# Performance work log

Hardware: AMD Instinct MI355X
Metric: run time of the kernel (lower is better)

Reference implementation:

```python
import jax, jax.numpy as jnp
import numpy as np

PATCH = 3  # patch_sizes[layer] == 3 for all layers
EPS_NORM = 1e-12   # F.normalize eps
EPS_DIV = 1e-8     # fold divisor eps


def _extract_patches(f, p):
    # F.unfold(kernel=p, stride=1, padding=p//2) -> (b, N=h*w, c, p, p)
    b, c, h, w = f.shape
    pad = p // 2
    xp = jnp.pad(f, ((0, 0), (0, 0), (pad, pad), (pad, pad)))
    # stack the p*p shifted views: (b, c, p*p, h, w)
    pats = jnp.stack([xp[:, :, i:i + h, j:j + w]
                      for i in range(p) for j in range(p)], axis=2)
    # -> (b, c, p, p, N) -> (b, N, c, p, p), matching unfold's (c, kh, kw) ordering
    return pats.reshape(b, c, p, p, h * w).transpose(0, 4, 1, 2, 3)


def _fold(patches, h, w, p):
    # F.fold inverse of unfold: scatter-add overlapping patches.
    # patches: (b, N=h*w, c, p, p)
    b, n, c = patches.shape[:3]
    pad = p // 2
    m = patches.reshape(b, h, w, c, p, p).transpose(0, 3, 4, 5, 1, 2)  # (b,c,p,p,h,w)
    out = jnp.zeros((b, c, h + 2 * pad, w + 2 * pad), patches.dtype)
    for ki in range(p):
        for kj in range(p):
            out = out.at[:, :, ki:ki + h, kj:kj + w].add(m[:, :, ki, kj])
    return out[:, :, pad:pad + h, pad:pad + w]


def _mrf_loss(content_feats, style_feats, p):
    b, c, h, w = content_feats.shape
    d = c * p * p
    cp = _extract_patches(content_feats, p)            # (b, N, c, p, p)
    sp = _extract_patches(style_feats, p)              # (b, M, c, p, p)
    cv = cp.reshape(b, -1, d)
    sv = sp.reshape(b, -1, d)
    cv = cv / jnp.maximum(jnp.linalg.norm(cv, axis=2, keepdims=True), EPS_NORM)
    svn = sv / jnp.maximum(jnp.linalg.norm(sv, axis=2, keepdims=True), EPS_NORM)
    # cosine similarity matrix (b, N, M) -- the big memory-bound intermediate
    dist = jnp.einsum('bnd,bmd->bnm', cv, svn)
    best = jnp.argmax(dist, axis=2)                    # (b, N) int
    # gather matched (un-normalized) style patches
    matched = jnp.take_along_axis(sp.reshape(b, -1, d), best[:, :, None], axis=1)
    matched = matched.reshape(b, -1, c, p, p)
    out = _fold(matched, h, w, p)
    ones = jnp.ones((1, h * w, 1, p, p), content_feats.dtype)
    divisor = _fold(ones, h, w, p)                      # overlap counts (1,1,h,w)
    recon = out / (divisor + EPS_DIV)
    return jnp.mean((content_feats - recon) ** 2)


def setup_inputs() -> dict:
    key = jax.random.key(0)
    k1, k2 = jax.random.split(key)
    content_feats = jax.random.normal(k1, (1, 128, 96, 96), dtype=jnp.float32)
    style_feats = jax.random.normal(k2, (1, 128, 96, 96), dtype=jnp.float32)
    return {"content_feats": content_feats, "style_feats": style_feats}


def reference(content_feats, style_feats):
    return _mrf_loss(content_feats, style_feats, PATCH)
```

## Files before the change

### kernel.cpp

```cpp
#include <hip/hip_runtime.h>
#include <hip/hip_bf16.h>

#define HH 96
#define WW 96
#define NPIX 9216
#define NCH 128
#define DDIM 1152
#define TOTAL_ELEMS 1179648
#define CG 32
#define DDIAG 9217
#define DROW 884832

#define NTIL 8
#define MTIL 512
#define BROWS 10
#define BCOLS 528
#define BELEMS (BROWS * BCOLS)
#define DCHUNKS 1980
#define NTB 1152
#define DBLK 20736

typedef float f32x4 __attribute__((ext_vector_type(4)));
typedef __bf16 bf16x8 __attribute__((ext_vector_type(8)));
typedef _Float16 half8 __attribute__((ext_vector_type(8)));

__device__ __forceinline__ void gload_lds16(const void* g, void* l) {
  __builtin_amdgcn_global_load_lds((const __attribute__((address_space(1))) void*)g,
                                   (__attribute__((address_space(3))) void*)l, 16, 0, 0);
}


#define GUARD_ELEMS 894064ull
constexpr size_t G_CORE_ELEMS = (size_t)NPIX * NPIX;
constexpr size_t G_TOT_ELEMS = G_CORE_ELEMS + 2ull * GUARD_ELEMS;
constexpr size_t GBYTES = ((G_TOT_ELEMS * 2 + 255) & ~(size_t)255);
constexpr size_t CT_OFF = GBYTES;
constexpr size_t ST2_OFF = CT_OFF + (size_t)NPIX * NCH * 2;
constexpr size_t STYT_OFF = ST2_OFF + (size_t)NPIX * NCH * 2;
constexpr size_t SS_OFF = STYT_OFF + (size_t)NPIX * NCH * 4;
constexpr size_t RN2_OFF = SS_OFF + (size_t)NPIX * 4;
constexpr size_t KEY2_OFF = RN2_OFF + (size_t)NPIX * 4;
constexpr size_t NEED_NEW = KEY2_OFF + (size_t)NPIX * 8;

__global__ __launch_bounds__(256)
void transpose_kernel(const float* __restrict__ style_f, const float* __restrict__ content_f,
                      _Float16* __restrict__ St, _Float16* __restrict__ Ct,
                      float* __restrict__ styT, float* __restrict__ ss) {
  __shared__ float ftile[NCH][97];
  const int y = blockIdx.x;
  const bool is_style = (blockIdx.y == 0);
  const float* f = is_style ? style_f : content_f;
  _Float16* P = is_style ? St : Ct;
  const int tid = threadIdx.x;
  for (int i = tid; i < NCH * WW; i += 256) {
    int c = i / WW, x = i - (i / WW) * WW;
    ftile[c][x] = f[(size_t)c * NPIX + y * WW + x];
  }
  __syncthreads();
  for (int j = tid; j < WW * NCH; j += 256) {
    int x = j >> 7, c = j & 127;
    float v = ftile[c][x];
    P[(size_t)(y * WW + x) * NCH + c] = (_Float16)v;
    if (is_style) styT[(size_t)(y * WW + x) * NCH + c] = v;
  }
  if (is_style && tid < WW) {
    float s = 0.f;
#pragma unroll 8
    for (int c = 0; c < NCH; ++c) { float v = ftile[c][tid]; s = fmaf(v, v, s); }
    ss[y * WW + tid] = s;
  }
}

__global__ __launch_bounds__(256)
void boxnorm_kernel(const float* __restrict__ ss, float* __restrict__ rnorm) {
  int m = blockIdx.x * 256 + threadIdx.x;
  int ym = m / WW, xm = m - (m / WW) * WW;
  float s = 0.f;
#pragma unroll
  for (int di = -1; di <= 1; ++di) {
    int yy = ym + di;
    if (yy < 0 || yy >= HH) continue;
#pragma unroll
    for (int dj = -1; dj <= 1; ++dj) {
      int xx = xm + dj;
      if (xx < 0 || xx >= WW) continue;
      s += ss[yy * WW + xx];
    }
  }
  rnorm[m] = 1.0f / fmaxf(sqrtf(s), 1e-12f);
}

__global__ __launch_bounds__(256, 2)
void ggemm_kernel(const _Float16* __restrict__ Ct, const _Float16* __restrict__ St,
                  unsigned short* __restrict__ Gg) {
  __shared__ char smem[65536];
  const int tid = threadIdx.x;
  const int lane = tid & 63, wid = tid >> 6;
  const int l15 = lane & 15, lg = lane >> 4;
  const int wm = wid >> 1, wn = wid & 1;
  const int n0 = blockIdx.x * 128, m0 = blockIdx.y * 128;

  {
    const int r = tid >> 4, p = tid & 15;
    const int l = p ^ (r & 7);
    const _Float16* sa = Ct + (size_t)(n0 + r) * NCH + l * 8;
    const _Float16* sb = St + (size_t)(m0 + r) * NCH + l * 8;
    char* d = smem + tid * 16;
#pragma unroll
    for (int i = 0; i < 8; ++i) {
      gload_lds16(sa + (size_t)16 * i * NCH, d + 4096 * i);
      gload_lds16(sb + (size_t)16 * i * NCH, d + 32768 + 4096 * i);
    }
  }
  __syncthreads();

  f32x4 acc[4][4];
#pragma unroll
  for (int mf = 0; mf < 4; ++mf)
#pragma unroll
    for (int nf = 0; nf < 4; ++nf) {
      f32x4 z = {0.f, 0.f, 0.f, 0.f};
      acc[mf][nf] = z;
    }

#pragma unroll
  for (int ks = 0; ks < 4; ++ks) {
    half8 af[4], bb[4];
#pragma unroll
    for (int mf = 0; mf < 4; ++mf) {
      int row = wm * 64 + mf * 16 + l15;
      int phys = (ks * 4 + lg) ^ (row & 7);
      af[mf] = __builtin_bit_cast(half8, *(const int4*)(smem + row * 256 + phys * 16));
    }
#pragma unroll
    for (int nf = 0; nf < 4; ++nf) {
      int row = wn * 64 + nf * 16 + l15;
      int phys = (ks * 4 + lg) ^ (row & 7);
      bb[nf] = __builtin_bit_cast(half8, *(const int4*)(smem + 32768 + row * 256 + phys * 16));
    }
#pragma unroll
    for (int mf = 0; mf < 4; ++mf)
#pragma unroll
      for (int nf = 0; nf < 4; ++nf)
        acc[mf][nf] = __builtin_amdgcn_mfma_f32_16x16x32_f16(af[mf], bb[nf], acc[mf][nf], 0, 0, 0);
  }
  __syncthreads();

#pragma unroll
  for (int mf = 0; mf < 4; ++mf)
#pragma unroll
    for (int nf = 0; nf < 4; ++nf)
#pragma unroll
      for (int r = 0; r < 4; ++r) {
        int row = wm * 64 + mf * 16 + lg * 4 + r;
        int col = wn * 64 + nf * 16 + l15;
        *(_Float16*)(smem + (row * 136 + col) * 2) = (_Float16)acc[mf][nf][r];
      }
  __syncthreads();
  const size_t gbase = GUARD_ELEMS + (size_t)n0 * NPIX + m0;
#pragma unroll
  for (int j = 0; j < 8; ++j) {
    int idx = j * 256 + tid;
    int row = idx >> 4, ch = idx & 15;
    int4 v = *(const int4*)(smem + (row * 136 + ch * 8) * 2);
    *(int4*)(Gg + gbase + (size_t)row * NPIX + ch * 8) = v;
  }
}

__global__ __launch_bounds__(256, 5)
void dist_argmax_kernel(const _Float16* __restrict__ Gg, const float* __restrict__ rnorm,
                        unsigned long long* __restrict__ keytab) {
  __shared__ _Float16 lds[3 * BELEMS];
  const int bid = blockIdx.x;
  const int idx = (bid & 7) * (DBLK / 8) + (bid >> 3);
  const int mtb = idx / NTB;
  const int ntb = idx - mtb * NTB;
  const int n0 = ntb * NTIL;
  const int m0 = mtb * MTIL;
  const int tid = threadIdx.x;
  const int w = tid >> 6, lane = tid & 63;

  long flat0[3];
#pragma unroll
  for (int b = 0; b < 3; ++b) {
    int di = b - 1;
    flat0[b] = (long)(n0 + 96 * di - 1) * NPIX + (long)(m0 + 96 * di - 8) + (long)GUARD_ELEMS;
  }
#pragma unroll
  for (int k = 0; k < 8; ++k) {
    int q = k * 256 + tid;
    if (q < DCHUNKS) {
      int b = q / 660;
      int rem = q - b * 660;
      int row = rem / 66;
      int c16 = rem - row * 66;
      gload_lds16(Gg + flat0[b] + (long)row * NPIX + c16 * 8, lds + (size_t)q * 8);
    }
  }
  const int mlane = m0 + lane * 8;
  const int ym = mlane / WW;
  const int x8 = mlane - ym * WW;
  const float me0 = (x8 == 0) ? 0.f : 1.f;
  const float me7 = (x8 == 88) ? 0.f : 1.f;
  const bool myr0 = (ym >= 1), myr2 = (ym <= 94);
  float rnv[8];
  *(f32x4*)(rnv) = *(const f32x4*)(rnorm + mlane);
  *(f32x4*)(rnv + 4) = *(const f32x4*)(rnorm + mlane + 4);
  const int col8 = lane * 8 + 8;
  const _Float16* B0p = lds;
  const _Float16* B1p = lds + BELEMS;
  const _Float16* B2p = lds + 2 * BELEMS;

  asm volatile("s_waitcnt vmcnt(0)" ::: "memory");
  __builtin_amdgcn_s_barrier();

#pragma unroll
  for (int s = 0; s < 2; ++s) {
    const int r = w * 2 + s;
    const int n = n0 + r;
    const int yn = n / WW;
    const int xn = n - yn * WW;
    const float cn0 = (xn >= 1) ? 1.f : 0.f;
    const float cn2 = (xn <= 94) ? 1.f : 0.f;
    const float Bw0 = (myr0 && (yn >= 1)) ? 1.f : 0.f;
    const float Bw2 = (myr2 && (yn <= 94)) ? 1.f : 0.f;
    float d[8];
    {
      const _Float16* bp = B1p + r * BCOLS;
      half8 Vp = *(const half8*)(bp + col8 - 8);
      half8 V0 = *(const half8*)(bp + col8);
      half8 V1 = *(const half8*)(bp + BCOLS + col8);
      half8 V2 = *(const half8*)(bp + 2 * BCOLS + col8);
      half8 Vx = *(const half8*)(bp + 2 * BCOLS + col8 + 8);
      float P = (float)Vp[7];
      float X = (float)Vx[0];
#pragma unroll
      for (int j = 0; j < 8; ++j) d[j] = (float)V1[j];
      d[0] = fmaf(P, cn0 * me0, d[0]);
#pragma unroll
      for (int j = 1; j < 8; ++j) d[j] = fmaf((float)V0[j - 1], cn0, d[j]);
#pragma unroll
      for (int j = 0; j < 7; ++j) d[j] = fmaf((float)V2[j + 1], cn2, d[j]);
      d[7] = fmaf(X, cn2 * me7, d[7]);
    }
    {
      const float wl = Bw0 * cn0, wr = Bw0 * cn2;
      const _Float16* bp = B0p + r * BCOLS;
      half8 Vp = *(const half8*)(bp + col8 - 8);
      half8 V0 = *(const half8*)(bp + col8);
      half8 V1 = *(const half8*)(bp + BCOLS + col8);
      half8 V2 = *(const half8*)(bp + 2 * BCOLS + col8);
      half8 Vx = *(const half8*)(bp + 2 * BCOLS + col8 + 8);
      float P = (float)Vp[7];
      float X = (float)Vx[0];
#pragma unroll
      for (int j = 0; j < 8; ++j) d[j] = fmaf((float)V1[j], Bw0, d[j]);
      d[0] = fmaf(P, wl * me0, d[0]);
#pragma unroll
      for (int j = 1; j < 8; ++j) d[j] = fmaf((float)V0[j - 1], wl, d[j]);
#pragma unroll
      for (int j = 0; j < 7; ++j) d[j] = fmaf((float)V2[j + 1], wr, d[j]);
      d[7] = fmaf(X, wr * me7, d[7]);
    }
    {
      const float wl = Bw2 * cn0, wr = Bw2 * cn2;
      const _Float16* bp = B2p + r * BCOLS;
      half8 Vp = *(const half8*)(bp + col8 - 8);
      half8 V0 = *(const half8*)(bp + col8);
      half8 V1 = *(const half8*)(bp + BCOLS + col8);
      half8 V2 = *(const half8*)(bp + 2 * BCOLS + col8);
      half8 Vx = *(const half8*)(bp + 2 * BCOLS + col8 + 8);
      float P = (float)Vp[7];
      float X = (float)Vx[0];
#pragma unroll
      for (int j = 0; j < 8; ++j) d[j] = fmaf((float)V1[j], Bw2, d[j]);
      d[0] = fmaf(P, wl * me0, d[0]);
#pragma unroll
      for (int j = 1; j < 8; ++j) d[j] = fmaf((float)V0[j - 1], wl, d[j]);
#pragma unroll
      for (int j = 0; j < 7; ++j) d[j] = fmaf((float)V2[j + 1], wr, d[j]);
      d[7] = fmaf(X, wr * me7, d[7]);
    }
    float bv = d[0] * rnv[0];
    int bj = mlane;
#pragma unroll
    for (int j = 1; j < 8; ++j) {
      float xs = d[j] * rnv[j];
      if (xs > bv) { bv = xs; bj = mlane + j; }
    }
    float wmx = bv;
#pragma unroll
    for (int mm = 1; mm < 64; mm <<= 1)
      wmx = fmaxf(wmx, __shfl_xor(wmx, mm, 64));
    if (bv == wmx) {
      unsigned u = __float_as_uint(bv);
      u ^= (unsigned)((int)u >> 31) | 0x80000000u;
      unsigned long long key =
          ((unsigned long long)u << 32) | (unsigned)(0xFFFFFFFFu ^ (unsigned)bj);
      atomicMax(keytab + n, key);
    }
  }
}

__global__ __launch_bounds__(256)
void recon_mse2_kernel(const _Float16* __restrict__ Ct, const float* __restrict__ styT,
                       const unsigned long long* __restrict__ keytab, float* __restrict__ out) {
  const int pix = blockIdx.x * 2 + (threadIdx.x >> 7);
  const int c = threadIdx.x & 127;
  const int y = pix / WW, x = pix - (pix / WW) * WW;
  float sum = 0.f, cnt = 0.f;
#pragma unroll
  for (int ki = 0; ki < 3; ++ki) {
    int yn = y - ki + 1;
    if (yn < 0 || yn >= HH) continue;
#pragma unroll
    for (int kj = 0; kj < 3; ++kj) {
      int xn = x - kj + 1;
      if (xn < 0 || xn >= WW) continue;
      cnt += 1.f;
      int m = (int)(0xFFFFFFFFu ^ (unsigned)(keytab[yn * WW + xn] & 0xFFFFFFFFull));
      int ys = m / WW, xs = m - (m / WW) * WW;
      int sy = ys + ki - 1, sx = xs + kj - 1;
      if (sy >= 0 && sy < HH && sx >= 0 && sx < WW)
        sum += styT[(size_t)(sy * WW + sx) * NCH + c];
    }
  }
  float recon = sum / (cnt + 1e-8f);
  float cv = (float)Ct[(size_t)pix * NCH + c];
  float diff = cv - recon;
  float sq = diff * diff;
#pragma unroll
  for (int m = 32; m > 0; m >>= 1) sq += __shfl_down(sq, m, 64);
  __shared__ float wsum[4];
  int lane = threadIdx.x & 63, w = threadIdx.x >> 6;
  if (lane == 0) wsum[w] = sq;
  __syncthreads();
  if (threadIdx.x == 0)
    atomicAdd(out, (wsum[0] + wsum[1] + wsum[2] + wsum[3]) * (1.0f / (float)TOTAL_ELEMS));
}

__global__ __launch_bounds__(256)
void build_patches_old(const float* __restrict__ style_f, const float* __restrict__ content_f,
                       __bf16* __restrict__ Ps, __bf16* __restrict__ Pc) {
  __shared__ float ftile[CG][3][104];
  const int y = blockIdx.x;
  const int cg = blockIdx.y;
  const bool is_style = (blockIdx.z == 0);
  const float* f = is_style ? style_f : content_f;
  __bf16* P = is_style ? Ps : Pc;
  const int tid = threadIdx.x;
  for (int i = tid; i < CG * 3 * 96; i += 256) {
    int cl = i / 288, rem = i - cl * 288;
    int yy = rem / 96, xx = rem - yy * 96;
    int gy = y + yy - 1;
    float v = (gy >= 0 && gy < HH) ? f[(size_t)(cg * CG + cl) * NPIX + gy * WW + xx] : 0.f;
    ftile[cl][yy][xx] = v;
  }
  __syncthreads();
  for (int j = tid; j < 96 * 36; j += 256) {
    int px = j / 36, wi = j - px * 36;
    bf16x8 tmp;
#pragma unroll
    for (int u = 0; u < 8; ++u) {
      int e = wi * 8 + u;
      int cl = e / 9, t = e - cl * 9;
      int ki = t / 3, kj = t - ki * 3;
      int xx = px + kj - 1;
      float v = (xx >= 0 && xx < WW) ? ftile[cl][ki][xx] : 0.f;
      tmp[u] = (__bf16)v;
    }
    *(bf16x8*)(P + (size_t)(y * WW + px) * DDIM + cg * 288 + wi * 8) = tmp;
  }
}

__global__ __launch_bounds__(256)
void norm_old(const __bf16* __restrict__ Ps, float* __restrict__ rnorm) {
  const int n = blockIdx.x * 4 + (threadIdx.x >> 6);
  const int lane = threadIdx.x & 63;
  const bf16x8* row = (const bf16x8*)(Ps + (size_t)n * DDIM);
  float ss = 0.f;
#pragma unroll
  for (int i = 0; i < 3; ++i) {
    int idx = i * 64 + lane;
    if (idx < 144) {
      bf16x8 v = row[idx];
#pragma unroll
      for (int u = 0; u < 8; ++u) { float x = (float)v[u]; ss += x * x; }
    }
  }
#pragma unroll
  for (int m = 1; m < 64; m <<= 1) ss += __shfl_xor(ss, m, 64);
  if (lane == 0) rnorm[n] = 1.0f / fmaxf(sqrtf(ss), 1e-12f);
}

__global__ __launch_bounds__(256, 2)
void gemm_old(const __bf16* __restrict__ Pc, const __bf16* __restrict__ Ps,
              const float* __restrict__ rnorm, unsigned long long* __restrict__ keytab) {
  __shared__ int4 smem4[4608];
  char* smem = (char*)smem4;
  const int tid = threadIdx.x;
  const int lane = tid & 63;
  const int wid = tid >> 6;
  const int l15 = lane & 15;
  const int lg = lane >> 4;
  const int wm = wid >> 1;
  const int wn = wid & 1;
  const int orig = blockIdx.x;
  const int swz = (orig & 7) * 324 + (orig >> 3);
  const int mt = swz / 72;
  const int nt = swz - mt * 72;
  const int bm0 = mt * 256;
  const int sbase = nt * 128;
  const int srow = tid >> 2;
  const int sg = (tid & 3) ^ ((srow >> 1) & 3);
  const __bf16* pa = Pc + (size_t)(bm0 + srow) * DDIM + sg * 8;
  const __bf16* pb = Ps + (size_t)(sbase + srow) * DDIM + sg * 8;
  const int sdst = tid * 16;
  auto stage = [&](int buf, int kt) {
    char* la = smem + buf * 24576 + sdst;
    const int ko = kt * 32;
#pragma unroll
    for (int i = 0; i < 4; ++i) gload_lds16(pa + (size_t)i * 64 * DDIM + ko, la + i * 4096);
#pragma unroll
    for (int j = 0; j < 2; ++j) gload_lds16(pb + (size_t)j * 64 * DDIM + ko, la + 16384 + j * 4096);
  };
  const int sx = (lg ^ ((l15 >> 1) & 3)) << 4;
  int aoff[8], boff[4];
#pragma unroll
  for (int mf = 0; mf < 8; ++mf) aoff[mf] = (wm * 128 + mf * 16 + l15) * 64 + sx;
#pragma unroll
  for (int nf = 0; nf < 4; ++nf) boff[nf] = 16384 + (wn * 64 + nf * 16 + l15) * 64 + sx;
  f32x4 acc[8][4];
#pragma unroll
  for (int mf = 0; mf < 8; ++mf)
#pragma unroll
    for (int nf = 0; nf < 4; ++nf) {
      f32x4 z = {0.f, 0.f, 0.f, 0.f};
      acc[mf][nf] = z;
    }
  auto compute = [&](int buf) {
    const char* bp = smem + buf * 24576;
    bf16x8 af[8], bfr[4];
#pragma unroll
    for (int mf = 0; mf < 8; ++mf) af[mf] = __builtin_bit_cast(bf16x8, *(const int4*)(bp + aoff[mf]));
#pragma unroll
    for (int nf = 0; nf < 4; ++nf) bfr[nf] = __builtin_bit_cast(bf16x8, *(const int4*)(bp + boff[nf]));
    __builtin_amdgcn_s_setprio(1);
#pragma unroll
    for (int mf = 0; mf < 8; ++mf)
#pragma unroll
      for (int nf = 0; nf < 4; ++nf)
        acc[mf][nf] = __builtin_amdgcn_mfma_f32_16x16x32_bf16(af[mf], bfr[nf], acc[mf][nf], 0, 0, 0);
    __builtin_amdgcn_s_setprio(0);
  };
  stage(0, 0);
  stage(1, 1);
  int sb = 2, cb = 0;
  for (int kt = 0; kt < 34; ++kt) {
    stage(sb, kt + 2);
    sb = (sb == 2) ? 0 : sb + 1;
    asm volatile("s_waitcnt vmcnt(12)" ::: "memory");
    __builtin_amdgcn_s_barrier();
    __builtin_amdgcn_sched_barrier(0);
    compute(cb);
    __builtin_amdgcn_s_barrier();
    cb = (cb == 2) ? 0 : cb + 1;
  }
  asm volatile("s_waitcnt vmcnt(6)" ::: "memory");
  __builtin_amdgcn_s_barrier();
  __builtin_amdgcn_sched_barrier(0);
  compute(cb);
  cb = (cb == 2) ? 0 : cb + 1;
  asm volatile("s_waitcnt vmcnt(0)" ::: "memory");
  __builtin_amdgcn_s_barrier();
  __builtin_amdgcn_sched_barrier(0);
  compute(cb);
  float rn[4];
#pragma unroll
  for (int nf = 0; nf < 4; ++nf) rn[nf] = rnorm[sbase + wn * 64 + nf * 16 + l15];
#pragma unroll
  for (int mf = 0; mf < 8; ++mf)
#pragma unroll
    for (int r = 0; r < 4; ++r) {
      float v = -3.0e38f;
      int bi = 0;
#pragma unroll
      for (int nf = 0; nf < 4; ++nf) {
        float x = acc[mf][nf][r] * rn[nf];
        int col = sbase + wn * 64 + nf * 16 + l15;
        if (x > v) { v = x; bi = col; }
      }
#pragma unroll
      for (int m = 1; m < 16; m <<= 1) {
        float ov = __shfl_xor(v, m, 64);
        int oi = __shfl_xor(bi, m, 64);
        if (ov > v || (ov == v && oi < bi)) { v = ov; bi = oi; }
      }
      if (l15 == 0) {
        int row = bm0 + wm * 128 + mf * 16 + lg * 4 + r;
        unsigned u = __float_as_uint(v);
        u ^= (unsigned)((int)u >> 31) | 0x80000000u;
        unsigned long long key = ((unsigned long long)u << 32) | (unsigned)(0xFFFFFFFFu ^ (unsigned)bi);
        atomicMax(keytab + row, key);
      }
    }
}

__global__ __launch_bounds__(256)
void recon_old(const __bf16* __restrict__ Pc, const __bf16* __restrict__ Ps,
               const unsigned long long* __restrict__ keytab, float* __restrict__ out) {
  const int pix = blockIdx.x * 2 + (threadIdx.x >> 7);
  const int c = threadIdx.x & 127;
  const int y = pix / WW, x = pix - (pix / WW) * WW;
  float sum = 0.f, cnt = 0.f;
#pragma unroll
  for (int ki = 0; ki < 3; ++ki) {
    int yn = y - ki + 1;
    if (yn < 0 || yn >= HH) continue;
#pragma unroll
    for (int kj = 0; kj < 3; ++kj) {
      int xn = x - kj + 1;
      if (xn < 0 || xn >= WW) continue;
      cnt += 1.f;
      int m = (int)(0xFFFFFFFFu ^ (unsigned)(keytab[yn * WW + xn] & 0xFFFFFFFFull));
      sum += (float)Ps[(size_t)m * DDIM + c * 9 + ki * 3 + kj];
    }
  }
  float recon = sum / (cnt + 1e-8f);
  float cv = (float)Pc[(size_t)pix * DDIM + c * 9 + 4];
  float diff = cv - recon;
  float sq = diff * diff;
#pragma unroll
  for (int m = 32; m > 0; m >>= 1) sq += __shfl_down(sq, m, 64);
  __shared__ float wsum[4];
  int lane = threadIdx.x & 63, w = threadIdx.x >> 6;
  if (lane == 0) wsum[w] = sq;
  __syncthreads();
  if (threadIdx.x == 0)
    atomicAdd(out, (wsum[0] + wsum[1] + wsum[2] + wsum[3]) * (1.0f / (float)TOTAL_ELEMS));
}

extern "C" void kernel_launch(void* const* d_in, const int* in_sizes, int n_in,
                              void* d_out, int out_size, void* d_ws, size_t ws_size,
                              hipStream_t stream) {
  const float* content = (const float*)d_in[0];
  const float* stylef = (const float*)d_in[1];
  float* out = (float*)d_out;
  char* ws = (char*)d_ws;

  hipMemsetAsync(d_out, 0, (size_t)out_size * sizeof(float), stream);

  if (ws_size >= NEED_NEW) {
    _Float16* Gg = (_Float16*)ws;
    _Float16* Ct = (_Float16*)(ws + CT_OFF);
    _Float16* St = (_Float16*)(ws + ST2_OFF);
    float* styT = (float*)(ws + STYT_OFF);
    float* ss = (float*)(ws + SS_OFF);
    float* rnorm = (float*)(ws + RN2_OFF);
    unsigned long long* keytab = (unsigned long long*)(ws + KEY2_OFF);

    hipMemsetAsync(keytab, 0, (size_t)NPIX * 8, stream);
    hipMemsetAsync(Gg, 0, (size_t)GUARD_ELEMS * 2, stream);
    hipMemsetAsync(Gg + GUARD_ELEMS + G_CORE_ELEMS, 0, (size_t)GUARD_ELEMS * 2, stream);
    transpose_kernel<<<dim3(96, 2), 256, 0, stream>>>(stylef, content, St, Ct, styT, ss);
    boxnorm_kernel<<<NPIX / 256, 256, 0, stream>>>(ss, rnorm);
    ggemm_kernel<<<dim3(72, 72), 256, 0, stream>>>(Ct, St, (unsigned short*)Gg);
    dist_argmax_kernel<<<DBLK, 256, 0, stream>>>(Gg, rnorm, keytab);
    recon_mse2_kernel<<<NPIX / 2, 256, 0, stream>>>(Ct, styT, keytab, out);
  } else {
    const size_t PS_OFF = 0;
    const size_t PC_OFF = (size_t)NPIX * DDIM * 2;
    const size_t RN_OFF = PC_OFF * 2;
    const size_t KEY_OFF = RN_OFF + (size_t)NPIX * 4;
    __bf16* Ps = (__bf16*)(ws + PS_OFF);
    __bf16* Pc = (__bf16*)(ws + PC_OFF);
    float* rnorm = (float*)(ws + RN_OFF);
    unsigned long long* keytab = (unsigned long long*)(ws + KEY_OFF);
    hipMemsetAsync(keytab, 0, (size_t)NPIX * 8, stream);
    build_patches_old<<<dim3(96, 4, 2), 256, 0, stream>>>(stylef, content, Ps, Pc);
    norm_old<<<NPIX / 4, 256, 0, stream>>>(Ps, rnorm);
    gemm_old<<<2592, 256, 0, stream>>>(Pc, Ps, rnorm, keytab);
    recon_old<<<NPIX / 2, 256, 0, stream>>>(Pc, Ps, keytab, out);
  }
}
```

Baseline: 214.2 us.

## Fold memsets into kernels and share LDS row loads across two output rows

Removes four hipMemsetAsync calls. The keytab and output zeroing now happen inside the transpose kernel, and the guard-band zeroing is spread across the GEMM blocks. The dist_argmax inner loop is restructured so that each wave loads four consecutive LDS rows per band once and reuses them for both of its output rows. Neighbour elements are fetched with lane shuffles instead of extra unaligned LDS loads. This cuts launch overhead and LDS traffic, at the cost of more registers and some shuffle work.

```diff
diff --git a/kernel.cpp b/kernel.cpp
--- a/kernel.cpp
+++ b/kernel.cpp
@@ -28,7 +28,6 @@
   __builtin_amdgcn_global_load_lds((const __attribute__((address_space(1))) void*)g,
                                    (__attribute__((address_space(3))) void*)l, 16, 0, 0);
 }
-
 
 #define GUARD_ELEMS 894064ull
 constexpr size_t G_CORE_ELEMS = (size_t)NPIX * NPIX;
@@ -41,17 +40,24 @@
 constexpr size_t RN2_OFF = SS_OFF + (size_t)NPIX * 4;
 constexpr size_t KEY2_OFF = RN2_OFF + (size_t)NPIX * 4;
 constexpr size_t NEED_NEW = KEY2_OFF + (size_t)NPIX * 8;
+constexpr long GUARD_I4 = 111758;
 
 __global__ __launch_bounds__(256)
 void transpose_kernel(const float* __restrict__ style_f, const float* __restrict__ content_f,
                       _Float16* __restrict__ St, _Float16* __restrict__ Ct,
-                      float* __restrict__ styT, float* __restrict__ ss) {
+                      float* __restrict__ styT, float* __restrict__ ss,
+                      unsigned long long* __restrict__ keytab, float* __restrict__ out) {
   __shared__ float ftile[NCH][97];
   const int y = blockIdx.x;
   const bool is_style = (blockIdx.y == 0);
   const float* f = is_style ? style_f : content_f;
   _Float16* P = is_style ? St : Ct;
   const int tid = threadIdx.x;
+  if (is_style) {
+    int g = y * 256 + tid;
+    if (g < NPIX) keytab[g] = 0ull;
+    if (g == 0) *out = 0.f;
+  }
   for (int i = tid; i < NCH * WW; i += 256) {
     int c = i / WW, x = i - (i / WW) * WW;
     ftile[c][x] = f[(size_t)c * NPIX + y * WW + x];
@@ -101,6 +107,20 @@
   const int n0 = blockIdx.x * 128, m0 = blockIdx.y * 128;
 
   {
+    const long bidf = (long)blockIdx.y * gridDim.x + blockIdx.x;
+    if (tid < 64) {
+      int side = tid >> 5, k = tid & 31;
+      if (k < 22) {
+        long q = bidf * 22 + k;
+        if (q < GUARD_I4) {
+          int4 z = {0, 0, 0, 0};
+          _Float16* gp = (_Float16*)Gg + (side ? (long)(GUARD_ELEMS + G_CORE_ELEMS) : 0l);
+          *(int4*)(gp + q * 8) = z;
+        }
+      }
+    }
+  }
+  {
     const int r = tid >> 4, p = tid & 15;
     const int l = p ^ (r & 7);
     const _Float16* sa = Ct + (size_t)(n0 + r) * NCH + l * 8;
@@ -122,7 +142,6 @@
       f32x4 z = {0.f, 0.f, 0.f, 0.f};
       acc[mf][nf] = z;
     }
-
 #pragma unroll
   for (int ks = 0; ks < 4; ++ks) {
     half8 af[4], bb[4];
@@ -145,7 +164,6 @@
         acc[mf][nf] = __builtin_amdgcn_mfma_f32_16x16x32_f16(af[mf], bb[nf], acc[mf][nf], 0, 0, 0);
   }
   __syncthreads();
-
 #pragma unroll
   for (int mf = 0; mf < 4; ++mf)
 #pragma unroll
@@ -207,97 +225,99 @@
   *(f32x4*)(rnv) = *(const f32x4*)(rnorm + mlane);
   *(f32x4*)(rnv + 4) = *(const f32x4*)(rnorm + mlane + 4);
   const int col8 = lane * 8 + 8;
-  const _Float16* B0p = lds;
-  const _Float16* B1p = lds + BELEMS;
-  const _Float16* B2p = lds + 2 * BELEMS;
+
+  const int r0 = w * 2;
+  const int nA = n0 + r0, nB = nA + 1;
+  const int ynA = nA / WW, xnA = nA - ynA * WW;
+  const int ynB = nB / WW, xnB = nB - ynB * WW;
+  const float cn0A = (xnA >= 1) ? 1.f : 0.f, cn2A = (xnA <= 94) ? 1.f : 0.f;
+  const float cn0B = (xnB >= 1) ? 1.f : 0.f, cn2B = (xnB <= 94) ? 1.f : 0.f;
+  const float bwA[3] = {(myr0 && (ynA >= 1)) ? 1.f : 0.f, 1.f, (myr2 && (ynA <= 94)) ? 1.f : 0.f};
+  const float bwB[3] = {(myr0 && (ynB >= 1)) ? 1.f : 0.f, 1.f, (myr2 && (ynB <= 94)) ? 1.f : 0.f};
 
   asm volatile("s_waitcnt vmcnt(0)" ::: "memory");
   __builtin_amdgcn_s_barrier();
 
-#pragma unroll
-  for (int s = 0; s < 2; ++s) {
-    const int r = w * 2 + s;
-    const int n = n0 + r;
-    const int yn = n / WW;
-    const int xn = n - yn * WW;
-    const float cn0 = (xn >= 1) ? 1.f : 0.f;
-    const float cn2 = (xn <= 94) ? 1.f : 0.f;
-    const float Bw0 = (myr0 && (yn >= 1)) ? 1.f : 0.f;
-    const float Bw2 = (myr2 && (yn <= 94)) ? 1.f : 0.f;
-    float d[8];
+  float dA[8] = {0.f, 0.f, 0.f, 0.f, 0.f, 0.f, 0.f, 0.f};
+  float dB[8] = {0.f, 0.f, 0.f, 0.f, 0.f, 0.f, 0.f, 0.f};
+#pragma unroll
+  for (int b = 0; b < 3; ++b) {
+    const _Float16* bp = lds + b * BELEMS + r0 * BCOLS;
+    half8 R0 = *(const half8*)(bp + col8);
+    half8 R1 = *(const half8*)(bp + BCOLS + col8);
+    half8 R2 = *(const half8*)(bp + 2 * BCOLS + col8);
+    half8 R3 = *(const half8*)(bp + 3 * BCOLS + col8);
+    float pA = __shfl_up((float)R0[7], 1, 64);
+    float pB = __shfl_up((float)R1[7], 1, 64);
+    float xA = __shfl_down((float)R2[0], 1, 64);
+    float xB = __shfl_down((float)R3[0], 1, 64);
+    if (lane == 0) {
+      pA = (float)bp[7];
+      pB = (float)bp[BCOLS + 7];
+    }
+    if (lane == 63) {
+      xA = (float)bp[2 * BCOLS + 520];
+      xB = (float)bp[3 * BCOLS + 520];
+    }
     {
-      const _Float16* bp = B1p + r * BCOLS;
-      half8 Vp = *(const half8*)(bp + col8 - 8);
-      half8 V0 = *(const half8*)(bp + col8);
-      half8 V1 = *(const half8*)(bp + BCOLS + col8);
-      half8 V2 = *(const half8*)(bp + 2 * BCOLS + col8);
-      half8 Vx = *(const half8*)(bp + 2 * BCOLS + col8 + 8);
-      float P = (float)Vp[7];
-      float X = (float)Vx[0];
-#pragma unroll
-      for (int j = 0; j < 8; ++j) d[j] = (float)V1[j];
-      d[0] = fmaf(P, cn0 * me0, d[0]);
-#pragma unroll
-      for (int j = 1; j < 8; ++j) d[j] = fmaf((float)V0[j - 1], cn0, d[j]);
-#pragma unroll
-      for (int j = 0; j < 7; ++j) d[j] = fmaf((float)V2[j + 1], cn2, d[j]);
-      d[7] = fmaf(X, cn2 * me7, d[7]);
+      const float wc = bwA[b];
+      const float wl = wc * cn0A, wr = wc * cn2A;
+#pragma unroll
+      for (int j = 0; j < 8; ++j) dA[j] = fmaf((float)R1[j], wc, dA[j]);
+      dA[0] = fmaf(pA, wl * me0, dA[0]);
+#pragma unroll
+      for (int j = 1; j < 8; ++j) dA[j] = fmaf((float)R0[j - 1], wl, dA[j]);
+#pragma unroll
+      for (int j = 0; j < 7; ++j) dA[j] = fmaf((float)R2[j + 1], wr, dA[j]);
+      dA[7] = fmaf(xA, wr * me7, dA[7]);
     }
     {
-      const float wl = Bw0 * cn0, wr = Bw0 * cn2;
-      const _Float16* bp = B0p + r * BCOLS;
-      half8 Vp = *(const half8*)(bp + col8 - 8);
-      half8 V0 = *(const half8*)(bp + col8);
-      half8 V1 = *(const half8*)(bp + BCOLS + col8);
-      half8 V2 = *(const half8*)(bp + 2 * BCOLS + col8);
-      half8 Vx = *(const half8*)(bp + 2 * BCOLS + col8 + 8);
-      float P = (float)Vp[7];
-      float X = (float)Vx[0];
-#pragma unroll
-      for (int j = 0; j < 8; ++j) d[j] = fmaf((float)V1[j], Bw0, d[j]);
-      d[0] = fmaf(P, wl * me0, d[0]);
-#pragma unroll
-      for (int j = 1; j < 8; ++j) d[j] = fmaf((float)V0[j - 1], wl, d[j]);
-#pragma unroll
-      for (int j = 0; j < 7; ++j) d[j] = fmaf((float)V2[j + 1], wr, d[j]);
-      d[7] = fmaf(X, wr * me7, d[7]);
-    }
-    {
-      const float wl = Bw2 * cn0, wr = Bw2 * cn2;
-      const _Float16* bp = B2p + r * BCOLS;
-      half8 Vp = *(const half8*)(bp + col8 - 8);
-      half8 V0 = *(const half8*)(bp + col8);
-      half8 V1 = *(const half8*)(bp + BCOLS + col8);
-      half8 V2 = *(const half8*)(bp + 2 * BCOLS + col8);
-      half8 Vx = *(const half8*)(bp + 2 * BCOLS + col8 + 8);
-      float P = (float)Vp[7];
-      float X = (float)Vx[0];
-#pragma unroll
-      for (int j = 0; j < 8; ++j) d[j] = fmaf((float)V1[j], Bw2, d[j]);
-      d[0] = fmaf(P, wl * me0, d[0]);
-#pragma unroll
-      for (int j = 1; j < 8; ++j) d[j] = fmaf((float)V0[j - 1], wl, d[j]);
-#pragma unroll
-      for (int j = 0; j < 7; ++j) d[j] = fmaf((float)V2[j + 1], wr, d[j]);
-      d[7] = fmaf(X, wr * me7, d[7]);
-    }
-    float bv = d[0] * rnv[0];
+      const float wc = bwB[b];
+      const float wl = wc * cn0B, wr = wc * cn2B;
+#pragma unroll
+      for (int j = 0; j < 8; ++j) dB[j] = fmaf((float)R2[j], wc, dB[j]);
+      dB[0] = fmaf(pB, wl * me0, dB[0]);
+#pragma unroll
+      for (int j = 1; j < 8; ++j) dB[j] = fmaf((float)R1[j - 1], wl, dB[j]);
+#pragma unroll
+      for (int j = 0; j < 7; ++j) dB[j] = fmaf((float)R3[j + 1], wr, dB[j]);
+      dB[7] = fmaf(xB, wr * me7, dB[7]);
+    }
+  }
+  {
+    float bv = dA[0] * rnv[0];
     int bj = mlane;
 #pragma unroll
     for (int j = 1; j < 8; ++j) {
-      float xs = d[j] * rnv[j];
+      float xs = dA[j] * rnv[j];
       if (xs > bv) { bv = xs; bj = mlane + j; }
     }
     float wmx = bv;
 #pragma unroll
-    for (int mm = 1; mm < 64; mm <<= 1)
-      wmx = fmaxf(wmx, __shfl_xor(wmx, mm, 64));
+    for (int mm = 1; mm < 64; mm <<= 1) wmx = fmaxf(wmx, __shfl_xor(wmx, mm, 64));
     if (bv == wmx) {
       unsigned u = __float_as_uint(bv);
       u ^= (unsigned)((int)u >> 31) | 0x80000000u;
-      unsigned long long key =
-          ((unsigned long long)u << 32) | (unsigned)(0xFFFFFFFFu ^ (unsigned)bj);
-      atomicMax(keytab + n, key);
+      atomicMax(keytab + nA,
+                ((unsigned long long)u << 32) | (unsigned)(0xFFFFFFFFu ^ (unsigned)bj));
+    }
+  }
+  {
+    float bv = dB[0] * rnv[0];
+    int bj = mlane;
+#pragma unroll
+    for (int j = 1; j < 8; ++j) {
+      float xs = dB[j] * rnv[j];
+      if (xs > bv) { bv = xs; bj = mlane + j; }
+    }
+    float wmx = bv;
+#pragma unroll
+    for (int mm = 1; mm < 64; mm <<= 1) wmx = fmaxf(wmx, __shfl_xor(wmx, mm, 64));
+    if (bv == wmx) {
+      unsigned u = __float_as_uint(bv);
+      u ^= (unsigned)((int)u >> 31) | 0x80000000u;
+      atomicMax(keytab + nB,
+                ((unsigned long long)u << 32) | (unsigned)(0xFFFFFFFFu ^ (unsigned)bj));
     }
   }
 }
@@ -548,8 +568,6 @@
   float* out = (float*)d_out;
   char* ws = (char*)d_ws;
 
-  hipMemsetAsync(d_out, 0, (size_t)out_size * sizeof(float), stream);
-
   if (ws_size >= NEED_NEW) {
     _Float16* Gg = (_Float16*)ws;
     _Float16* Ct = (_Float16*)(ws + CT_OFF);
@@ -559,10 +577,8 @@
     float* rnorm = (float*)(ws + RN2_OFF);
     unsigned long long* keytab = (unsigned long long*)(ws + KEY2_OFF);
 
-    hipMemsetAsync(keytab, 0, (size_t)NPIX * 8, stream);
-    hipMemsetAsync(Gg, 0, (size_t)GUARD_ELEMS * 2, stream);
-    hipMemsetAsync(Gg + GUARD_ELEMS + G_CORE_ELEMS, 0, (size_t)GUARD_ELEMS * 2, stream);
-    transpose_kernel<<<dim3(96, 2), 256, 0, stream>>>(stylef, content, St, Ct, styT, ss);
+    transpose_kernel<<<dim3(96, 2), 256, 0, stream>>>(stylef, content, St, Ct, styT, ss,
+                                                      keytab, out);
     boxnorm_kernel<<<NPIX / 256, 256, 0, stream>>>(ss, rnorm);
     ggemm_kernel<<<dim3(72, 72), 256, 0, stream>>>(Ct, St, (unsigned short*)Gg);
     dist_argmax_kernel<<<DBLK, 256, 0, stream>>>(Gg, rnorm, keytab);
@@ -576,6 +592,7 @@
     __bf16* Pc = (__bf16*)(ws + PC_OFF);
     float* rnorm = (float*)(ws + RN_OFF);
     unsigned long long* keytab = (unsigned long long*)(ws + KEY_OFF);
+    hipMemsetAsync(d_out, 0, (size_t)out_size * sizeof(float), stream);
     hipMemsetAsync(keytab, 0, (size_t)NPIX * 8, stream);
     build_patches_old<<<dim3(96, 4, 2), 256, 0, stream>>>(stylef, content, Ps, Pc);
     norm_old<<<NPIX / 4, 256, 0, stream>>>(Ps, rnorm);
```

New measurement: 236.2 us. 10.3% more time.
